# Kernel optimization log

Measured on AMD Instinct MI355X. Metric: run time of the kernel, lower is better.

The kernel has to match this reference:

```python
import jax, jax.numpy as jnp
import numpy as np

B, G = 32, 8          # batch, num_genres
N, T = 64, 64         # notes_size, timestep_size (input)
D, O = 32, 32         # notes_out, timestep_out (output)


def setup_inputs() -> dict:
    key = jax.random.key(0)
    k1, k2, k3, k4, k5 = jax.random.split(key, 5)
    x = jax.random.normal(k1, (B, N, T), dtype=jnp.float32)
    y = jax.random.uniform(k2, (B, G), dtype=jnp.float32)
    weight = jax.random.normal(k3, (G, D, O, N, T), dtype=jnp.float32) * 0.02
    bias = jax.random.normal(k4, (D * O,), dtype=jnp.float32) * 0.02
    mask = jax.random.randint(k5, (O, T), 0, 2).astype(jnp.float32)
    return {"x": x, "y": y, "weight": weight, "bias": bias, "mask": mask}


def reference(x, y, weight, bias, mask):
    # Fused form of:
    #   mw  = einsum('gdont,ot->gdont', weight, mask)
    #   mw2 = einsum('gdont,bg->bdont', mw, y)      # huge intermediate avoided
    #   out = einsum('bnt,bdont->bdo', x, mw2) + bias
    mw = weight * mask[None, None, :, None, :]          # (g,d,o,n,t)
    xw = jnp.einsum('bnt,gdont->bgdo', x, mw)           # contract n,t first
    out = jnp.einsum('bg,bgdo->bdo', y, xw)             # (b,d,o)
    return out + bias.reshape(D, O)[None, :, :]
```

## Files before the change

### kernel.cpp

```cpp
#include <hip/hip_runtime.h>
#include <hip/hip_bf16.h>

typedef __bf16 bf16x8 __attribute__((ext_vector_type(8)));
typedef float f32x4 __attribute__((ext_vector_type(4)));

#define G 8
#define B 32
#define D 32
#define O 32
#define K 4096
#define T 64
#define KSPLIT 2
#define KCHUNK (K / KSPLIT)
#define BK 256
#define NSTEP (KCHUNK / BK)
#define NKT (K / 32)

#define XMT_ELEMS (O * B * K)
#define S_ELEMS   (KSPLIT * G * O * D * B)

__global__ __launch_bounds__(256) void prep_xmt(const float* __restrict__ x,
                                                const float* __restrict__ mask,
                                                __bf16* __restrict__ xmt) {
    int tid = blockIdx.x * 256 + threadIdx.x;
    int o  = tid >> 14;
    int kt = (tid >> 7) & 127;
    int b  = (tid >> 2) & 31;
    int c  = tid & 3;
    int k  = kt * 32 + c * 8;
    int t  = k & 63;
    const float4 x0 = *(const float4*)(x + b * K + k);
    const float4 x1 = *(const float4*)(x + b * K + k + 4);
    const float4 m0 = *(const float4*)(mask + o * T + t);
    const float4 m1 = *(const float4*)(mask + o * T + t + 4);
    bf16x8 r;
    r[0] = (__bf16)(x0.x * m0.x); r[1] = (__bf16)(x0.y * m0.y);
    r[2] = (__bf16)(x0.z * m0.z); r[3] = (__bf16)(x0.w * m0.w);
    r[4] = (__bf16)(x1.x * m1.x); r[5] = (__bf16)(x1.y * m1.y);
    r[6] = (__bf16)(x1.z * m1.z); r[7] = (__bf16)(x1.w * m1.w);
    *(bf16x8*)(xmt + (size_t)tid * 8) = r;
}

__global__ __launch_bounds__(256) void gemm_main(const float* __restrict__ W,
                                                 const __bf16* __restrict__ xmt,
                                                 float* __restrict__ S) {
    __shared__ float ldsW[2][32 * BK];
    const int o  = blockIdx.x, g = blockIdx.y, ks = blockIdx.z;
    const int wid  = threadIdx.x >> 6;
    const int lane = threadIdx.x & 63;
    const int bh = wid & 1, dh = wid >> 1;
    const int l15 = lane & 15, g16 = lane >> 4;

    const int r = dh * 16 + l15;
    const int lds_ro = r * 1024 + ((g16 * 32) ^ ((r & 7) * 16));

    const __bf16* xb = xmt + ((size_t)o * 128 + ks * 64) * 1024
                           + (bh * 16 + l15) * 32 + g16 * 8;

    const size_t wrow0 = ((size_t)(g * D + 8 * wid) * O + o) * K + (size_t)ks * KCHUNK;

    f32x4 acc = {0.f, 0.f, 0.f, 0.f};

#define STAGE(buf, step)                                                          \
    {                                                                             \
        _Pragma("unroll")                                                         \
        for (int i = 0; i < 8; ++i) {                                             \
            const int d = 8 * wid + i;                                            \
            const char* src = (const char*)(W + wrow0 + (size_t)i * (O * K)       \
                                            + (size_t)(step) * BK)                \
                              + ((lane * 16) ^ ((d & 7) * 16));                   \
            __builtin_amdgcn_global_load_lds(                                     \
                (const __attribute__((address_space(1))) void*)src,               \
                (__attribute__((address_space(3))) void*)((char*)&ldsW[buf][0]    \
                                                          + d * 1024),            \
                16, 0, 0);                                                        \
        }                                                                         \
    }

    STAGE(0, 0);
    __syncthreads();

    int cur = 0;
    for (int step = 0; step < NSTEP; ++step) {
        if (step + 1 < NSTEP) STAGE(cur ^ 1, step + 1);

        const char* lb = (const char*)&ldsW[cur][0];
        const __bf16* xs = xb + (size_t)(step * 8) * 1024;
        #pragma unroll
        for (int s = 0; s < 8; ++s) {
            const int a0 = lds_ro + s * 128;
            const f32x4 alo = *(const f32x4*)(lb + a0);
            const f32x4 ahi = *(const f32x4*)(lb + (a0 ^ 16));
            bf16x8 af;
            af[0] = (__bf16)alo[0]; af[1] = (__bf16)alo[1];
            af[2] = (__bf16)alo[2]; af[3] = (__bf16)alo[3];
            af[4] = (__bf16)ahi[0]; af[5] = (__bf16)ahi[1];
            af[6] = (__bf16)ahi[2]; af[7] = (__bf16)ahi[3];
            const bf16x8 bfr = *(const bf16x8*)(xs + (size_t)s * 1024);
            acc = __builtin_amdgcn_mfma_f32_16x16x32_bf16(af, bfr, acc, 0, 0, 0);
        }
        __syncthreads();
        cur ^= 1;
    }
#undef STAGE

    float* Sp = S + (((size_t)(ks * G + g) * O + o) * D + dh * 16) * B + bh * 16;
    #pragma unroll
    for (int i = 0; i < 4; ++i)
        Sp[(g16 * 4 + i) * B + l15] = acc[i];
}

__global__ __launch_bounds__(256) void reduce_out(const float* __restrict__ S,
                                                  const float* __restrict__ y,
                                                  const float* __restrict__ bias,
                                                  float* __restrict__ out) {
    int tid = blockIdx.x * 256 + threadIdx.x;
    int o = tid >> 10, d = (tid >> 5) & 31, b = tid & 31;
    float acc = bias[d * O + o];
    #pragma unroll
    for (int g = 0; g < G; ++g) {
        float s = S[(size_t)g * (O * D * B) + tid]
                + S[(size_t)(G + g) * (O * D * B) + tid];
        acc += y[b * G + g] * s;
    }
    out[b * (D * O) + d * O + o] = acc;
}

extern "C" void kernel_launch(void* const* d_in, const int* in_sizes, int n_in,
                              void* d_out, int out_size, void* d_ws, size_t ws_size,
                              hipStream_t stream) {
    const float* x    = (const float*)d_in[0];
    const float* y    = (const float*)d_in[1];
    const float* w    = (const float*)d_in[2];
    const float* bias = (const float*)d_in[3];
    const float* mask = (const float*)d_in[4];
    float* out = (float*)d_out;

    __bf16* xmt = (__bf16*)d_ws;
    float*  S   = (float*)((char*)d_ws + (size_t)XMT_ELEMS * sizeof(__bf16));

    prep_xmt<<<2048, 256, 0, stream>>>(x, mask, xmt);
    gemm_main<<<dim3(O, G, KSPLIT), 256, 0, stream>>>(w, xmt, S);
    reduce_out<<<128, 256, 0, stream>>>(S, y, bias, out);
}
```

Before: 36.72 us.

## Apply mask to weights in GEMM and drop per-o masked x copies

The GEMM grid now runs over d instead of o, so each block's 32 rows are different o values. The mask can then be applied to the weight fragment in registers before the bf16 conversion. The prep kernel shrinks from writing a masked bf16 copy of x for every o (32x replicated) to a single bf16 cast of x. This removes most of the prep kernel's writes and the GEMM's reads of that large buffer, at the cost of extra multiplies per MFMA fragment. The W load pattern and the S layout change to match the new grid.

```diff
diff --git a/kernel.cpp b/kernel.cpp
--- a/kernel.cpp
+++ b/kernel.cpp
@@ -14,50 +14,49 @@
 #define KCHUNK (K / KSPLIT)
 #define BK 256
 #define NSTEP (KCHUNK / BK)
-#define NKT (K / 32)
 
-#define XMT_ELEMS (O * B * K)
-#define S_ELEMS   (KSPLIT * G * O * D * B)
+#define XB_ELEMS (B * K)
+#define S_ELEMS  (KSPLIT * G * D * O * B)
 
-__global__ __launch_bounds__(256) void prep_xmt(const float* __restrict__ x,
-                                                const float* __restrict__ mask,
-                                                __bf16* __restrict__ xmt) {
+__global__ __launch_bounds__(256) void prep_xb(const float* __restrict__ x,
+                                               __bf16* __restrict__ xb) {
     int tid = blockIdx.x * 256 + threadIdx.x;
-    int o  = tid >> 14;
-    int kt = (tid >> 7) & 127;
+    int kt = tid >> 7;
     int b  = (tid >> 2) & 31;
     int c  = tid & 3;
     int k  = kt * 32 + c * 8;
-    int t  = k & 63;
     const float4 x0 = *(const float4*)(x + b * K + k);
     const float4 x1 = *(const float4*)(x + b * K + k + 4);
-    const float4 m0 = *(const float4*)(mask + o * T + t);
-    const float4 m1 = *(const float4*)(mask + o * T + t + 4);
     bf16x8 r;
-    r[0] = (__bf16)(x0.x * m0.x); r[1] = (__bf16)(x0.y * m0.y);
-    r[2] = (__bf16)(x0.z * m0.z); r[3] = (__bf16)(x0.w * m0.w);
-    r[4] = (__bf16)(x1.x * m1.x); r[5] = (__bf16)(x1.y * m1.y);
-    r[6] = (__bf16)(x1.z * m1.z); r[7] = (__bf16)(x1.w * m1.w);
-    *(bf16x8*)(xmt + (size_t)tid * 8) = r;
+    r[0] = (__bf16)x0.x; r[1] = (__bf16)x0.y; r[2] = (__bf16)x0.z; r[3] = (__bf16)x0.w;
+    r[4] = (__bf16)x1.x; r[5] = (__bf16)x1.y; r[6] = (__bf16)x1.z; r[7] = (__bf16)x1.w;
+    *(bf16x8*)(xb + (size_t)tid * 8) = r;
 }
 
 __global__ __launch_bounds__(256) void gemm_main(const float* __restrict__ W,
-                                                 const __bf16* __restrict__ xmt,
+                                                 const __bf16* __restrict__ xb,
+                                                 const float* __restrict__ mask,
                                                  float* __restrict__ S) {
     __shared__ float ldsW[2][32 * BK];
-    const int o  = blockIdx.x, g = blockIdx.y, ks = blockIdx.z;
+    const int d  = blockIdx.x, g = blockIdx.y, ks = blockIdx.z;
     const int wid  = threadIdx.x >> 6;
     const int lane = threadIdx.x & 63;
-    const int bh = wid & 1, dh = wid >> 1;
+    const int bh = wid & 1, oh = wid >> 1;
     const int l15 = lane & 15, g16 = lane >> 4;
 
-    const int r = dh * 16 + l15;
+    const int r = oh * 16 + l15;
     const int lds_ro = r * 1024 + ((g16 * 32) ^ ((r & 7) * 16));
 
-    const __bf16* xb = xmt + ((size_t)o * 128 + ks * 64) * 1024
+    const float* mrow = mask + r * T + g16 * 8;
+    const float4 me0 = *(const float4*)(mrow);
+    const float4 me1 = *(const float4*)(mrow + 4);
+    const float4 mo0 = *(const float4*)(mrow + 32);
+    const float4 mo1 = *(const float4*)(mrow + 36);
+
+    const __bf16* xbl = xb + (size_t)(ks * (KCHUNK / 32)) * 1024
                            + (bh * 16 + l15) * 32 + g16 * 8;
 
-    const size_t wrow0 = ((size_t)(g * D + 8 * wid) * O + o) * K + (size_t)ks * KCHUNK;
+    const size_t wrow0 = ((size_t)(g * D + d) * O + 8 * wid) * K + (size_t)ks * KCHUNK;
 
     f32x4 acc = {0.f, 0.f, 0.f, 0.f};
 
@@ -65,14 +64,14 @@
     {                                                                             \
         _Pragma("unroll")                                                         \
         for (int i = 0; i < 8; ++i) {                                             \
-            const int d = 8 * wid + i;                                            \
-            const char* src = (const char*)(W + wrow0 + (size_t)i * (O * K)       \
+            const int row = 8 * wid + i;                                          \
+            const char* src = (const char*)(W + wrow0 + (size_t)i * K             \
                                             + (size_t)(step) * BK)                \
-                              + ((lane * 16) ^ ((d & 7) * 16));                   \
+                              + ((lane * 16) ^ (i * 16));                         \
             __builtin_amdgcn_global_load_lds(                                     \
                 (const __attribute__((address_space(1))) void*)src,               \
                 (__attribute__((address_space(3))) void*)((char*)&ldsW[buf][0]    \
-                                                          + d * 1024),            \
+                                                          + row * 1024),          \
                 16, 0, 0);                                                        \
         }                                                                         \
     }
@@ -85,17 +84,19 @@
         if (step + 1 < NSTEP) STAGE(cur ^ 1, step + 1);
 
         const char* lb = (const char*)&ldsW[cur][0];
-        const __bf16* xs = xb + (size_t)(step * 8) * 1024;
+        const __bf16* xs = xbl + (size_t)(step * 8) * 1024;
         #pragma unroll
         for (int s = 0; s < 8; ++s) {
             const int a0 = lds_ro + s * 128;
             const f32x4 alo = *(const f32x4*)(lb + a0);
             const f32x4 ahi = *(const f32x4*)(lb + (a0 ^ 16));
+            const float4 ms0 = (s & 1) ? mo0 : me0;
+            const float4 ms1 = (s & 1) ? mo1 : me1;
             bf16x8 af;
-            af[0] = (__bf16)alo[0]; af[1] = (__bf16)alo[1];
-            af[2] = (__bf16)alo[2]; af[3] = (__bf16)alo[3];
-            af[4] = (__bf16)ahi[0]; af[5] = (__bf16)ahi[1];
-            af[6] = (__bf16)ahi[2]; af[7] = (__bf16)ahi[3];
+            af[0] = (__bf16)(alo[0] * ms0.x); af[1] = (__bf16)(alo[1] * ms0.y);
+            af[2] = (__bf16)(alo[2] * ms0.z); af[3] = (__bf16)(alo[3] * ms0.w);
+            af[4] = (__bf16)(ahi[0] * ms1.x); af[5] = (__bf16)(ahi[1] * ms1.y);
+            af[6] = (__bf16)(ahi[2] * ms1.z); af[7] = (__bf16)(ahi[3] * ms1.w);
             const bf16x8 bfr = *(const bf16x8*)(xs + (size_t)s * 1024);
             acc = __builtin_amdgcn_mfma_f32_16x16x32_bf16(af, bfr, acc, 0, 0, 0);
         }
@@ -104,7 +105,7 @@
     }
 #undef STAGE
 
-    float* Sp = S + (((size_t)(ks * G + g) * O + o) * D + dh * 16) * B + bh * 16;
+    float* Sp = S + (((size_t)(ks * G + g) * D + d) * O + oh * 16) * B + bh * 16;
     #pragma unroll
     for (int i = 0; i < 4; ++i)
         Sp[(g16 * 4 + i) * B + l15] = acc[i];
@@ -115,12 +116,12 @@
                                                   const float* __restrict__ bias,
                                                   float* __restrict__ out) {
     int tid = blockIdx.x * 256 + threadIdx.x;
-    int o = tid >> 10, d = (tid >> 5) & 31, b = tid & 31;
+    int d = tid >> 10, o = (tid >> 5) & 31, b = tid & 31;
     float acc = bias[d * O + o];
     #pragma unroll
     for (int g = 0; g < G; ++g) {
-        float s = S[(size_t)g * (O * D * B) + tid]
-                + S[(size_t)(G + g) * (O * D * B) + tid];
+        float s = S[(size_t)g * (D * O * B) + tid]
+                + S[(size_t)(G + g) * (D * O * B) + tid];
         acc += y[b * G + g] * s;
     }
     out[b * (D * O) + d * O + o] = acc;
@@ -136,10 +137,10 @@
     const float* mask = (const float*)d_in[4];
     float* out = (float*)d_out;
 
-    __bf16* xmt = (__bf16*)d_ws;
-    float*  S   = (float*)((char*)d_ws + (size_t)XMT_ELEMS * sizeof(__bf16));
+    __bf16* xbp = (__bf16*)d_ws;
+    float*  S   = (float*)((char*)d_ws + (size_t)XB_ELEMS * sizeof(__bf16));
 
-    prep_xmt<<<2048, 256, 0, stream>>>(x, mask, xmt);
-    gemm_main<<<dim3(O, G, KSPLIT), 256, 0, stream>>>(w, xmt, S);
+    prep_xb<<<64, 256, 0, stream>>>(x, xbp);
+    gemm_main<<<dim3(D, G, KSPLIT), 256, 0, stream>>>(w, xbp, mask, S);
     reduce_out<<<128, 256, 0, stream>>>(S, y, bias, out);
 }
```

After: 36.54 us. About the same (-0.5%).
